# Kernel tuning notes

Hardware: AMD Instinct MI355X
Metric: run time of the kernel (lower is better)

The kernel has to match this reference:

```python
import jax, jax.numpy as jnp
import numpy as np

B, S, D = 512, 500, 128
NQ, NC, NQD, NCD = 10000, 500, 100, 100

def _glorot(key, shape):
    fan_in, fan_out = shape[0], shape[1]
    lim = np.sqrt(6.0 / (fan_in + fan_out))
    return jax.random.uniform(key, shape, jnp.float32, -lim, lim)

def setup_inputs() -> dict:
    key = jax.random.key(0)
    ks = jax.random.split(key, 24)
    inp = {
        'question_seq': jax.random.randint(ks[0], (B, S), 0, NQ),
        'concept_seq': jax.random.randint(ks[1], (B, S), 0, NC),
        'question_diff_seq': jax.random.randint(ks[2], (B, S), 0, NQD),
        'concept_diff_seq': jax.random.randint(ks[3], (B, S), 0, NCD),
        'correct_seq': jax.random.randint(ks[4], (B, S), 0, 2),
        # embedding tables
        'Eq': jax.random.normal(ks[5], (NQ, D), jnp.float32),
        'Ec': jax.random.normal(ks[6], (NC, D), jnp.float32),
        'Eqd': jax.random.normal(ks[7], (NQD, D), jnp.float32),
        'Ecd': jax.random.normal(ks[8], (NCD, D), jnp.float32),
        'Ecorr': jax.random.normal(ks[9], (2, D), jnp.float32),
        # linear layers (stored as [in, out], y = x @ W + b)
        'Wx': _glorot(ks[10], (4 * D, D)), 'bx': jnp.zeros((D,), jnp.float32),
        'Wsdf1': _glorot(ks[11], (D, D)), 'bsdf1': jnp.zeros((D,), jnp.float32),
        'Wsdf2': _glorot(ks[12], (D, D)), 'bsdf2': jnp.zeros((D,), jnp.float32),
        'Wpka1': _glorot(ks[13], (2 * D, D)), 'bpka1': jnp.zeros((D,), jnp.float32),
        'Wpka2': _glorot(ks[14], (2 * D, D)), 'bpka2': jnp.zeros((D,), jnp.float32),
        'Wki': _glorot(ks[15], (4 * D, D)), 'bki': jnp.zeros((D,), jnp.float32),
        # xavier_uniform init of h_pre (torch nn.init.xavier_uniform_ on zeros(B, D))
        'h0': _glorot(ks[16], (B, D)),
    }
    return inp

def reference(question_seq, concept_seq, question_diff_seq, concept_diff_seq,
              correct_seq, Eq, Ec, Eqd, Ecd, Ecorr, Wx, bx,
              Wsdf1, bsdf1, Wsdf2, bsdf2, Wpka1, bpka1, Wpka2, bpka2,
              Wki, bki, h0):
    # embed all sequences: [B, S, D]
    qe = Eq[question_seq]
    ce = Ec[concept_seq]
    qde = Eqd[question_diff_seq]
    cde = Ecd[concept_diff_seq]
    co = Ecorr[correct_seq]
    # x_t = generate_x_MLP(concat(...)) precomputed for all timesteps
    x_all = jnp.concatenate([qe, ce, qde, cde], axis=-1) @ Wx + bx  # [B, S, D]

    # time-major slices for scan over t = 0 .. S-2
    tm = lambda a: jnp.swapaxes(a, 0, 1)  # [S, B, D]
    xs = (tm(x_all)[:-1], tm(x_all)[1:], tm(co)[:-1], tm(qde)[:-1], tm(cde)[:-1])

    def step(h_pre, inputs):
        x_t, x_next, co_t, qd_t, cd_t = inputs
        input_sdf = x_t - h_pre
        sdf = jax.nn.sigmoid(input_sdf @ Wsdf1 + bsdf1) * jnp.tanh(input_sdf @ Wsdf2 + bsdf2)
        input_pka = jnp.concatenate([sdf, co_t], axis=-1)
        pka = jax.nn.sigmoid(input_pka @ Wpka1 + bpka1) * jnp.tanh(input_pka @ Wpka2 + bpka2)
        input_ki = jnp.concatenate([h_pre, co_t, qd_t, cd_t], axis=-1)
        gamma = jax.nn.sigmoid(input_ki @ Wki + bki)
        h = gamma * h_pre + (1.0 - gamma) * pka
        y_t = jax.nn.sigmoid(jnp.sum(x_next * h, axis=-1))  # [B]
        return h, y_t

    _, ys = jax.lax.scan(step, h0, xs)  # ys: [S-1, B]
    # y[:, S-1] is never written in the original (stays 0)
    y = jnp.concatenate([ys.T, jnp.zeros((question_seq.shape[0], 1), jnp.float32)], axis=1)
    return y
```

## Files before the change

### kernel.cpp

```cpp
#include <hip/hip_runtime.h>
#include <hip/hip_bf16.h>
#include <cstdint>
#include <cstddef>

#define BB 512
#define SS 500
#define TT 499
#define NRB 256
#define L2E 1.4426950408889634f

typedef float  f32x4  __attribute__((ext_vector_type(4)));
typedef short  bf16x8 __attribute__((ext_vector_type(8)));

static constexpr size_t OFF_TXQ   = 0;
static constexpr size_t OFF_TXC   = 5120000;
static constexpr size_t OFF_TXQD  = 5376000;
static constexpr size_t OFF_TXCD  = 5427200;
static constexpr size_t OFF_TKIQD = 5478400;
static constexpr size_t OFF_TKICD = 5529600;
static constexpr size_t OFF_TKICO = 5580800;
static constexpr size_t OFF_TP1   = 5581824;
static constexpr size_t OFF_TP2   = 5582848;
static constexpr size_t OFF_TXQ2  = 5583872;
static constexpr size_t OFF_TXC2  = 10703872;
static constexpr size_t OFF_WFRAG = 10959872;
static constexpr size_t OFF_CPK   = 11123712;
static constexpr size_t OFF_XCD   = 11254784;
static constexpr size_t OFF_KIPRE = 143375360;
static constexpr size_t OFF_YPART = 275495936;
static constexpr size_t TOTAL_WS  = 283671552;

__device__ unsigned char g_fb[TOTAL_WS];

__device__ __forceinline__ unsigned short f2bf(float f) {
    union { float f; uint32_t u; } v; v.f = f;
    uint32_t u = v.u;
    uint32_t r = u + 0x7FFFu + ((u >> 16) & 1u);
    return (unsigned short)(r >> 16);
}
__device__ __forceinline__ float fsig(float z) {
    return __builtin_amdgcn_rcpf(1.0f + __expf(-z));
}
__device__ __forceinline__ uint32_t cvtpk(float lo, float hi) {
    uint32_t r;
    asm("v_cvt_pk_bf16_f32 %0, %1, %2" : "=v"(r) : "v"(lo), "v"(hi));
    return r;
}
__device__ __forceinline__ void bar_lgkm() {
    asm volatile("s_waitcnt lgkmcnt(0)" ::: "memory");
    __builtin_amdgcn_s_barrier();
}
__device__ __forceinline__ float sum16(float x) {
    int a = __float_as_int(x);
    int b = __builtin_amdgcn_update_dpp(a, a, 0xB1, 0xF, 0xF, false);
    float s = x + __int_as_float(b);
    int c = __float_as_int(s);
    int d = __builtin_amdgcn_update_dpp(c, c, 0x4E, 0xF, 0xF, false);
    s += __int_as_float(d);
    int e = __float_as_int(s);
    int f = __builtin_amdgcn_update_dpp(e, e, 0x141, 0xF, 0xF, false);
    s += __int_as_float(f);
    int gg = __float_as_int(s);
    int hh = __builtin_amdgcn_update_dpp(gg, gg, 0x140, 0xF, 0xF, false);
    return s + __int_as_float(hh);
}

__global__ __launch_bounds__(128) void k_tables(
    const float* __restrict__ Eq, const float* __restrict__ Ec,
    const float* __restrict__ Eqd, const float* __restrict__ Ecd,
    const float* __restrict__ Ecorr,
    const float* __restrict__ Wx,  const float* __restrict__ bx,
    const float* __restrict__ Wpka1, const float* __restrict__ bpka1,
    const float* __restrict__ Wpka2, const float* __restrict__ bpka2,
    const float* __restrict__ Wki, const float* __restrict__ bki,
    float* __restrict__ Txq, float* __restrict__ Txc,
    float* __restrict__ Txqd, float* __restrict__ Txcd,
    float* __restrict__ TkiQd, float* __restrict__ TkiCd, float* __restrict__ TkiCo,
    float* __restrict__ Tp1, float* __restrict__ Tp2)
{
    int blk = blockIdx.x;
    const float* A; const float* W; const float* bias = nullptr; float* out; int row;
    float oscale = 1.0f;
    if      (blk < 10000) { A = Eq;    row = blk;          W = Wx;              bias = bx;    out = Txq;  }
    else if (blk < 10500) { A = Ec;    row = blk - 10000;  W = Wx  + 128*128;                 out = Txc;  }
    else if (blk < 10600) { A = Eqd;   row = blk - 10500;  W = Wx  + 256*128;                 out = Txqd; }
    else if (blk < 10700) { A = Ecd;   row = blk - 10600;  W = Wx  + 384*128;                 out = Txcd; }
    else if (blk < 10800) { A = Eqd;   row = blk - 10700;  W = Wki + 256*128;                 out = TkiQd;}
    else if (blk < 10900) { A = Ecd;   row = blk - 10800;  W = Wki + 384*128;                 out = TkiCd;}
    else if (blk < 10902) { A = Ecorr; row = blk - 10900;  W = Wki + 128*128;   bias = bki;   out = TkiCo;}
    else if (blk < 10904) { A = Ecorr; row = blk - 10902;  W = Wpka1 + 128*128; bias = bpka1; out = Tp1;  oscale = -L2E; }
    else                  { A = Ecorr; row = blk - 10904;  W = Wpka2 + 128*128; bias = bpka2; out = Tp2;  oscale = -2.0f*L2E; }

    __shared__ float a[128];
    int c = threadIdx.x;
    a[c] = A[row * 128 + c];
    __syncthreads();
    float acc = bias ? bias[c] : 0.0f;
    #pragma unroll 8
    for (int k = 0; k < 128; ++k) acc += a[k] * W[k * 128 + c];
    out[row * 128 + c] = acc * oscale;
}

__global__ __launch_bounds__(128) void k_tables2(
    const float* __restrict__ Wki,
    const float* __restrict__ Txq, const float* __restrict__ Txc,
    const float* __restrict__ Txqd, const float* __restrict__ Txcd,
    float* __restrict__ Txq2, float* __restrict__ Txc2,
    float* __restrict__ TkiQd, float* __restrict__ TkiCd)
{
    int blk = blockIdx.x;
    const float* A; float* out; int row; bool accum;
    if      (blk < 10000) { A = Txq;  row = blk;          out = Txq2;  accum = false; }
    else if (blk < 10500) { A = Txc;  row = blk - 10000;  out = Txc2;  accum = false; }
    else if (blk < 10600) { A = Txqd; row = blk - 10500;  out = TkiQd; accum = true;  }
    else                  { A = Txcd; row = blk - 10600;  out = TkiCd; accum = true;  }
    __shared__ float a[128];
    int c = threadIdx.x;
    a[c] = A[row * 128 + c];
    __syncthreads();
    float acc = accum ? out[row * 128 + c] : 0.0f;
    #pragma unroll 8
    for (int k = 0; k < 128; ++k) acc += a[k] * Wki[k * 128 + c];
    out[row * 128 + c] = acc;
}

__global__ __launch_bounds__(64) void k_wfrag(
    const float* __restrict__ Wsdf1, const float* __restrict__ Wsdf2,
    const float* __restrict__ Wpka1, const float* __restrict__ Wpka2,
    const float* __restrict__ Wki, unsigned short* __restrict__ wfrag)
{
    int bid = blockIdx.x;
    int m = bid >> 5, w = (bid >> 2) & 7, kt = bid & 3;
    const float* W = (m == 0) ? Wsdf1 : (m == 1) ? Wsdf2 : (m == 2) ? Wpka1 : (m == 3) ? Wpka2 : Wki;
    float sgn = (m == 0) ? -L2E : (m == 1) ? -2.0f*L2E : (m == 2) ? -L2E : (m == 3) ? -2.0f*L2E : L2E;
    int l = threadIdx.x;
    int cc = w * 16 + (l & 15);
    int k0 = kt * 32 + ((l >> 4) << 3);
    unsigned short v[8];
    #pragma unroll
    for (int j = 0; j < 8; ++j) v[j] = f2bf(sgn * W[(size_t)(k0 + j) * 128 + cc]);
    unsigned short* dst = wfrag + ((( (size_t)m * 8 + w) * 4 + kt) * 64 + l) * 8;
    #pragma unroll
    for (int j = 0; j < 8; ++j) dst[j] = v[j];
}

__global__ __launch_bounds__(256) void k_gather(
    const int* __restrict__ qs, const int* __restrict__ cs,
    const int* __restrict__ qds, const int* __restrict__ cds, const int* __restrict__ corr,
    const float* __restrict__ Txq, const float* __restrict__ Txc,
    const float* __restrict__ Txqd, const float* __restrict__ Txcd,
    const float* __restrict__ Txq2, const float* __restrict__ Txc2,
    const float* __restrict__ TkiQd, const float* __restrict__ TkiCd, const float* __restrict__ TkiCo,
    float* __restrict__ xcd, float* __restrict__ kipre, unsigned char* __restrict__ cpk)
{
    int bid = blockIdx.x;
    int t = bid >> 8, rb = bid & 255;
    int tid = threadIdx.x;
    int row = tid >> 7;
    int col = tid & 127;
    int b = rb * 2 + row;

    int iq  = qs  [(size_t)b * SS + t];
    int ic  = cs  [(size_t)b * SS + t];
    int iqd = qds [(size_t)b * SS + t];
    int icd = cds [(size_t)b * SS + t];
    int ico = corr[(size_t)b * SS + t];

    float x = Txq [(size_t)iq  * 128 + col] + Txc [(size_t)ic  * 128 + col]
            + Txqd[(size_t)iqd * 128 + col] + Txcd[(size_t)icd * 128 + col];
    float k = (Txq2 [(size_t)iq  * 128 + col] + Txc2 [(size_t)ic  * 128 + col]
             + TkiQd[(size_t)iqd * 128 + col] + TkiCd[(size_t)icd * 128 + col]
             + TkiCo[(size_t)ico * 128 + col]) * (-L2E);

    xcd  [(size_t)bid * 256 + tid] = x;
    kipre[(size_t)bid * 256 + tid] = k;

    if (tid == 0) {
        unsigned char bpk = 0;
        #pragma unroll
        for (int r = 0; r < 2; ++r)
            bpk |= (unsigned char)((corr[(size_t)(rb * 2 + r) * SS + t] & 1) << r);
        cpk[(size_t)rb * 512 + t] = bpk;
    }
}

__global__ __launch_bounds__(512, 2) void k_rec(
    const float* __restrict__ xcd, const float* __restrict__ kipre,
    const unsigned char* __restrict__ cpkg,
    const unsigned short* __restrict__ wfrag,
    const float* __restrict__ Tp1, const float* __restrict__ Tp2,
    const float* __restrict__ bsdf1, const float* __restrict__ bsdf2,
    const float* __restrict__ h0, float* __restrict__ ypart)
{
    int rb = blockIdx.x;
    int tid = threadIdx.x;
    int w = tid >> 6, l = tid & 63;
    int g = l >> 4, cl = l & 15;
    int col = w * 16 + cl;
    int row = g & 1;
    bool owner = (g < 2);

    __shared__ __align__(16) unsigned short dbuf[256];
    __shared__ __align__(16) unsigned short sbuf[256];

    bf16x8 wf[5][4];
    #pragma unroll
    for (int m = 0; m < 5; ++m)
        #pragma unroll
        for (int kt = 0; kt < 4; ++kt)
            wf[m][kt] = *(const bf16x8*)(wfrag + ((((size_t)m * 8 + w) * 4 + kt) * 64 + l) * 8);

    float bs1 = bsdf1[col] * (-L2E);
    float bs2 = bsdf2[col] * (-2.0f * L2E);
    float tp1a = Tp1[col], tp1b = Tp1[128 + col];
    float tp2a = Tp2[col], tp2b = Tp2[128 + col];

    float h = h0[(size_t)(rb * 2 + row) * 128 + col];

    char* pdw = (char*)dbuf + row * 256 + ((col * 2) ^ (row << 6));
    char* psw = (char*)sbuf + row * 256 + ((col * 2) ^ (row << 6));
    const bf16x8* prd[4]; const bf16x8* prs[4];
    int rrow = cl & 1;
    #pragma unroll
    for (int kt = 0; kt < 4; ++kt) {
        int off = rrow * 256 + ((kt * 64 + g * 16) ^ (rrow << 6));
        prd[kt] = (const bf16x8*)((char*)dbuf + off);
        prs[kt] = (const bf16x8*)((char*)sbuf + off);
    }

    const size_t TSTR = (size_t)NRB * 256;
    int eidx = row * 128 + col;
    const float* xp = xcd + (size_t)rb * 256 + eidx;
    const float* kp = kipre + (size_t)rb * 256 + eidx;
    const unsigned char* cp = cpkg + (size_t)rb * 512;

    float xn   = xp[TSTR];
    float xn2  = xp[2 * TSTR];
    float kip  = kp[0];
    float kip1 = kp[TSTR];
    unsigned char c0 = cp[0], c1v = cp[1];

    float* ypt = ypart + (size_t)rb * 16 + w * 2 + row;
    const size_t YSTR = (size_t)NRB * 16;
    bool ystore = (owner && cl == 0);

    {
        float x0 = xp[0];
        uint32_t pk = cvtpk(x0 - h, x0 - h);
        if (owner) *(unsigned short*)pdw = (unsigned short)pk;
    }
    bar_lgkm();

    #pragma unroll 2
    for (int t = 0; t < TT; ++t) {
        float xn3  = xp[(size_t)(t + 3) * TSTR];
        float kip2 = kp[(size_t)(t + 2) * TSTR];
        unsigned char c2v = cp[t + 2];

        f32x4 s1a = {bs1, bs1, bs1, bs1}, s1b = {0.f, 0.f, 0.f, 0.f};
        f32x4 s2a = {bs2, bs2, bs2, bs2}, s2b = {0.f, 0.f, 0.f, 0.f};
        f32x4 gda = {0.f, 0.f, 0.f, 0.f}, gdb = {0.f, 0.f, 0.f, 0.f};
        {
            bf16x8 d0 = *prd[0], d1 = *prd[1], d2 = *prd[2], d3 = *prd[3];
            s1a = __builtin_amdgcn_mfma_f32_16x16x32_bf16(d0, wf[0][0], s1a, 0, 0, 0);
            s2a = __builtin_amdgcn_mfma_f32_16x16x32_bf16(d0, wf[1][0], s2a, 0, 0, 0);
            gda = __builtin_amdgcn_mfma_f32_16x16x32_bf16(d0, wf[4][0], gda, 0, 0, 0);
            s1b = __builtin_amdgcn_mfma_f32_16x16x32_bf16(d2, wf[0][2], s1b, 0, 0, 0);
            s2b = __builtin_amdgcn_mfma_f32_16x16x32_bf16(d2, wf[1][2], s2b, 0, 0, 0);
            gdb = __builtin_amdgcn_mfma_f32_16x16x32_bf16(d2, wf[4][2], gdb, 0, 0, 0);
            s1a = __builtin_amdgcn_mfma_f32_16x16x32_bf16(d1, wf[0][1], s1a, 0, 0, 0);
            s2a = __builtin_amdgcn_mfma_f32_16x16x32_bf16(d1, wf[1][1], s2a, 0, 0, 0);
            gda = __builtin_amdgcn_mfma_f32_16x16x32_bf16(d1, wf[4][1], gda, 0, 0, 0);
            s1b = __builtin_amdgcn_mfma_f32_16x16x32_bf16(d3, wf[0][3], s1b, 0, 0, 0);
            s2b = __builtin_amdgcn_mfma_f32_16x16x32_bf16(d3, wf[1][3], s2b, 0, 0, 0);
            gdb = __builtin_amdgcn_mfma_f32_16x16x32_bf16(d3, wf[4][3], gdb, 0, 0, 0);
        }
        float s1v = (row ? s1a[1] : s1a[0]) + (row ? s1b[1] : s1b[0]);
        float s2v = (row ? s2a[1] : s2a[0]) + (row ? s2b[1] : s2b[0]);
        float gdv = (row ? gda[1] : gda[0]) + (row ? gdb[1] : gdb[0]);
        float gv = __builtin_amdgcn_rcpf(1.0f + __builtin_amdgcn_exp2f(gdv + kip));
        float e1 = __builtin_amdgcn_exp2f(s1v), e2 = __builtin_amdgcn_exp2f(s2v);
        float sdf = (1.0f - e2) * __builtin_amdgcn_rcpf((1.0f + e1) * (1.0f + e2));
        {
            uint32_t pk = cvtpk(sdf, sdf);
            if (owner) *(unsigned short*)psw = (unsigned short)pk;
        }
        bar_lgkm();

        f32x4 p1a = {0.f, 0.f, 0.f, 0.f}, p1b = {0.f, 0.f, 0.f, 0.f};
        f32x4 p2a = {0.f, 0.f, 0.f, 0.f}, p2b = {0.f, 0.f, 0.f, 0.f};
        {
            bf16x8 f0 = *prs[0], f1 = *prs[1], f2 = *prs[2], f3 = *prs[3];
            p1a = __builtin_amdgcn_mfma_f32_16x16x32_bf16(f0, wf[2][0], p1a, 0, 0, 0);
            p2a = __builtin_amdgcn_mfma_f32_16x16x32_bf16(f0, wf[3][0], p2a, 0, 0, 0);
            p1b = __builtin_amdgcn_mfma_f32_16x16x32_bf16(f2, wf[2][2], p1b, 0, 0, 0);
            p2b = __builtin_amdgcn_mfma_f32_16x16x32_bf16(f2, wf[3][2], p2b, 0, 0, 0);
            p1a = __builtin_amdgcn_mfma_f32_16x16x32_bf16(f1, wf[2][1], p1a, 0, 0, 0);
            p2a = __builtin_amdgcn_mfma_f32_16x16x32_bf16(f1, wf[3][1], p2a, 0, 0, 0);
            p1b = __builtin_amdgcn_mfma_f32_16x16x32_bf16(f3, wf[2][3], p1b, 0, 0, 0);
            p2b = __builtin_amdgcn_mfma_f32_16x16x32_bf16(f3, wf[3][3], p2b, 0, 0, 0);
        }
        float p1v = (row ? p1a[1] : p1a[0]) + (row ? p1b[1] : p1b[0]);
        float p2v = (row ? p2a[1] : p2a[0]) + (row ? p2b[1] : p2b[0]);
        unsigned int myb = (((unsigned int)c0) >> row) & 1u;
        float t1 = myb ? tp1b : tp1a;
        float t2 = myb ? tp2b : tp2a;
        float e1p = __builtin_amdgcn_exp2f(p1v + t1), e2p = __builtin_amdgcn_exp2f(p2v + t2);
        float pka = (1.0f - e2p) * __builtin_amdgcn_rcpf((1.0f + e1p) * (1.0f + e2p));
        h = gv * (h - pka) + pka;

        {
            uint32_t pk = cvtpk(xn - h, xn - h);
            if (owner) *(unsigned short*)pdw = (unsigned short)pk;
        }
        float yv = sum16(xn * h);
        if (ystore) ypt[0] = yv;
        ypt += YSTR;
        bar_lgkm();

        xn = xn2; xn2 = xn3; kip = kip1; kip1 = kip2; c0 = c1v; c1v = c2v;
    }
}

__global__ __launch_bounds__(256) void k_yfinal(const float* __restrict__ ypart, float* __restrict__ y)
{
    int id = blockIdx.x * 256 + threadIdx.x;
    if (id >= BB * SS) return;
    int b = id / SS, t = id - b * SS;
    if (t == TT) { y[id] = 0.0f; return; }
    int rb = b >> 1, r = b & 1;
    const float* base = ypart + (size_t)t * NRB * 16 + (size_t)rb * 16 + r;
    float s = 0.0f;
    #pragma unroll
    for (int w = 0; w < 8; ++w) s += base[w * 2];
    y[id] = fsig(s);
}

extern "C" void kernel_launch(void* const* d_in, const int* in_sizes, int n_in,
                              void* d_out, int out_size, void* d_ws, size_t ws_size,
                              hipStream_t stream) {
    const int* qs    = (const int*)d_in[0];
    const int* cs    = (const int*)d_in[1];
    const int* qds   = (const int*)d_in[2];
    const int* cds   = (const int*)d_in[3];
    const int* corr  = (const int*)d_in[4];
    const float* Eq    = (const float*)d_in[5];
    const float* Ec    = (const float*)d_in[6];
    const float* Eqd   = (const float*)d_in[7];
    const float* Ecd   = (const float*)d_in[8];
    const float* Ecorr = (const float*)d_in[9];
    const float* Wx    = (const float*)d_in[10];
    const float* bx    = (const float*)d_in[11];
    const float* Wsdf1 = (const float*)d_in[12];
    const float* bsdf1 = (const float*)d_in[13];
    const float* Wsdf2 = (const float*)d_in[14];
    const float* bsdf2 = (const float*)d_in[15];
    const float* Wpka1 = (const float*)d_in[16];
    const float* bpka1 = (const float*)d_in[17];
    const float* Wpka2 = (const float*)d_in[18];
    const float* bpka2 = (const float*)d_in[19];
    const float* Wki   = (const float*)d_in[20];
    const float* bki   = (const float*)d_in[21];
    const float* h0    = (const float*)d_in[22];

    char* base;
    if (ws_size >= TOTAL_WS) {
        base = (char*)d_ws;
    } else {
        void* p = nullptr;
        hipGetSymbolAddress(&p, HIP_SYMBOL(g_fb));
        base = (char*)p;
    }

    float* Txq   = (float*)(base + OFF_TXQ);
    float* Txc   = (float*)(base + OFF_TXC);
    float* Txqd  = (float*)(base + OFF_TXQD);
    float* Txcd  = (float*)(base + OFF_TXCD);
    float* TkiQd = (float*)(base + OFF_TKIQD);
    float* TkiCd = (float*)(base + OFF_TKICD);
    float* TkiCo = (float*)(base + OFF_TKICO);
    float* Tp1   = (float*)(base + OFF_TP1);
    float* Tp2   = (float*)(base + OFF_TP2);
    float* Txq2  = (float*)(base + OFF_TXQ2);
    float* Txc2  = (float*)(base + OFF_TXC2);
    unsigned short* wfrag = (unsigned short*)(base + OFF_WFRAG);
    unsigned char*  cpk   = (unsigned char*)(base + OFF_CPK);
    float* xcd   = (float*)(base + OFF_XCD);
    float* kipre = (float*)(base + OFF_KIPRE);
    float* ypart = (float*)(base + OFF_YPART);

    k_tables<<<10906, 128, 0, stream>>>(Eq, Ec, Eqd, Ecd, Ecorr, Wx, bx,
                                        Wpka1, bpka1, Wpka2, bpka2, Wki, bki,
                                        Txq, Txc, Txqd, Txcd, TkiQd, TkiCd, TkiCo, Tp1, Tp2);
    k_tables2<<<10700, 128, 0, stream>>>(Wki, Txq, Txc, Txqd, Txcd, Txq2, Txc2, TkiQd, TkiCd);
    k_wfrag<<<160, 64, 0, stream>>>(Wsdf1, Wsdf2, Wpka1, Wpka2, Wki, wfrag);
    k_gather<<<SS * NRB, 256, 0, stream>>>(qs, cs, qds, cds, corr,
                                           Txq, Txc, Txqd, Txcd, Txq2, Txc2,
                                           TkiQd, TkiCd, TkiCo, xcd, kipre, cpk);
    k_rec<<<NRB, 512, 0, stream>>>(xcd, kipre, cpk, wfrag, Tp1, Tp2,
                                   bsdf1, bsdf2, h0, ypart);
    k_yfinal<<<(BB * SS + 255) / 256, 256, 0, stream>>>(ypart, (float*)d_out);
}
```

Baseline: 550.0 us.

## Skew the two batch rows by half a step so their phases overlap

The recurrence kernel now handles its two batch rows as separate streams, A and B, offset by half a timestep. In each barrier-delimited phase, one row's sdf/gate matmuls run next to the other row's pka matmuls, and each row has its own LDS buffers. The aim is to give each phase independent MFMA and transcendental chains to interleave, hiding latency in the serial per-step dependency. The cost is that each MFMA now carries only one meaningful row instead of packing both, so MFMA count per step roughly doubles, and the loop unroll drops to 1.

```diff
diff --git a/kernel.cpp b/kernel.cpp
--- a/kernel.cpp
+++ b/kernel.cpp
@@ -11,6 +11,8 @@
 
 typedef float  f32x4  __attribute__((ext_vector_type(4)));
 typedef short  bf16x8 __attribute__((ext_vector_type(8)));
+
+#define MFMA16(A, B, C) __builtin_amdgcn_mfma_f32_16x16x32_bf16((A), (B), (C), 0, 0, 0)
 
 static constexpr size_t OFF_TXQ   = 0;
 static constexpr size_t OFF_TXC   = 5120000;
@@ -197,11 +199,13 @@
     int w = tid >> 6, l = tid & 63;
     int g = l >> 4, cl = l & 15;
     int col = w * 16 + cl;
-    int row = g & 1;
-    bool owner = (g < 2);
-
-    __shared__ __align__(16) unsigned short dbuf[256];
-    __shared__ __align__(16) unsigned short sbuf[256];
+    bool owner = (g == 0);
+    bool ystore = (l == 0);
+
+    __shared__ __align__(16) unsigned short dbufA[128];
+    __shared__ __align__(16) unsigned short sbufA[128];
+    __shared__ __align__(16) unsigned short dbufB[128];
+    __shared__ __align__(16) unsigned short sbufB[128];
 
     bf16x8 wf[5][4];
     #pragma unroll
@@ -215,110 +219,160 @@
     float tp1a = Tp1[col], tp1b = Tp1[128 + col];
     float tp2a = Tp2[col], tp2b = Tp2[128 + col];
 
-    float h = h0[(size_t)(rb * 2 + row) * 128 + col];
-
-    char* pdw = (char*)dbuf + row * 256 + ((col * 2) ^ (row << 6));
-    char* psw = (char*)sbuf + row * 256 + ((col * 2) ^ (row << 6));
-    const bf16x8* prd[4]; const bf16x8* prs[4];
-    int rrow = cl & 1;
-    #pragma unroll
-    for (int kt = 0; kt < 4; ++kt) {
-        int off = rrow * 256 + ((kt * 64 + g * 16) ^ (rrow << 6));
-        prd[kt] = (const bf16x8*)((char*)dbuf + off);
-        prs[kt] = (const bf16x8*)((char*)sbuf + off);
-    }
+    float hA = h0[(size_t)(rb * 2 + 0) * 128 + col];
+    float hB = h0[(size_t)(rb * 2 + 1) * 128 + col];
+
+    char* pdwA = (char*)dbufA + col * 2;
+    char* pswA = (char*)sbufA + col * 2;
+    char* pdwB = (char*)dbufB + col * 2;
+    char* pswB = (char*)sbufB + col * 2;
+    const char* rdA = (const char*)dbufA + g * 16;
+    const char* rsA = (const char*)sbufA + g * 16;
+    const char* rdB = (const char*)dbufB + g * 16;
+    const char* rsB = (const char*)sbufB + g * 16;
 
     const size_t TSTR = (size_t)NRB * 256;
-    int eidx = row * 128 + col;
-    const float* xp = xcd + (size_t)rb * 256 + eidx;
-    const float* kp = kipre + (size_t)rb * 256 + eidx;
+    const float* xpA = xcd + (size_t)rb * 256 + col;
+    const float* xpB = xpA + 128;
+    const float* kpA = kipre + (size_t)rb * 256 + col;
+    const float* kpB = kpA + 128;
     const unsigned char* cp = cpkg + (size_t)rb * 512;
 
-    float xn   = xp[TSTR];
-    float xn2  = xp[2 * TSTR];
-    float kip  = kp[0];
-    float kip1 = kp[TSTR];
-    unsigned char c0 = cp[0], c1v = cp[1];
-
-    float* ypt = ypart + (size_t)rb * 16 + w * 2 + row;
+    float xA0 = xpA[0], xB0 = xpB[0];
+    float kipA0 = kpA[0];
+    float kipB0 = kpB[0];
+    float xA1 = xpA[TSTR], xB1 = xpB[TSTR];
+    float kipB1 = kpB[TSTR];
+    unsigned char cpk0 = cp[0];
+    unsigned int cA0 = cpk0 & 1u, cB0 = (cpk0 >> 1) & 1u;
+
+    float* yptA = ypart + ((size_t)rb * 8 + w) * 2;
+    float* yptB = yptA + 1;
     const size_t YSTR = (size_t)NRB * 16;
-    bool ystore = (owner && cl == 0);
-
-    {
-        float x0 = xp[0];
-        uint32_t pk = cvtpk(x0 - h, x0 - h);
-        if (owner) *(unsigned short*)pdw = (unsigned short)pk;
+
+    if (owner) {
+        *(unsigned short*)pdwA = (unsigned short)cvtpk(xA0 - hA, xA0 - hA);
+        *(unsigned short*)pdwB = (unsigned short)cvtpk(xB0 - hB, xB0 - hB);
     }
     bar_lgkm();
-
-    #pragma unroll 2
-    for (int t = 0; t < TT; ++t) {
-        float xn3  = xp[(size_t)(t + 3) * TSTR];
-        float kip2 = kp[(size_t)(t + 2) * TSTR];
-        unsigned char c2v = cp[t + 2];
-
-        f32x4 s1a = {bs1, bs1, bs1, bs1}, s1b = {0.f, 0.f, 0.f, 0.f};
-        f32x4 s2a = {bs2, bs2, bs2, bs2}, s2b = {0.f, 0.f, 0.f, 0.f};
-        f32x4 gda = {0.f, 0.f, 0.f, 0.f}, gdb = {0.f, 0.f, 0.f, 0.f};
-        {
-            bf16x8 d0 = *prd[0], d1 = *prd[1], d2 = *prd[2], d3 = *prd[3];
-            s1a = __builtin_amdgcn_mfma_f32_16x16x32_bf16(d0, wf[0][0], s1a, 0, 0, 0);
-            s2a = __builtin_amdgcn_mfma_f32_16x16x32_bf16(d0, wf[1][0], s2a, 0, 0, 0);
-            gda = __builtin_amdgcn_mfma_f32_16x16x32_bf16(d0, wf[4][0], gda, 0, 0, 0);
-            s1b = __builtin_amdgcn_mfma_f32_16x16x32_bf16(d2, wf[0][2], s1b, 0, 0, 0);
-            s2b = __builtin_amdgcn_mfma_f32_16x16x32_bf16(d2, wf[1][2], s2b, 0, 0, 0);
-            gdb = __builtin_amdgcn_mfma_f32_16x16x32_bf16(d2, wf[4][2], gdb, 0, 0, 0);
-            s1a = __builtin_amdgcn_mfma_f32_16x16x32_bf16(d1, wf[0][1], s1a, 0, 0, 0);
-            s2a = __builtin_amdgcn_mfma_f32_16x16x32_bf16(d1, wf[1][1], s2a, 0, 0, 0);
-            gda = __builtin_amdgcn_mfma_f32_16x16x32_bf16(d1, wf[4][1], gda, 0, 0, 0);
-            s1b = __builtin_amdgcn_mfma_f32_16x16x32_bf16(d3, wf[0][3], s1b, 0, 0, 0);
-            s2b = __builtin_amdgcn_mfma_f32_16x16x32_bf16(d3, wf[1][3], s2b, 0, 0, 0);
-            gdb = __builtin_amdgcn_mfma_f32_16x16x32_bf16(d3, wf[4][3], gdb, 0, 0, 0);
-        }
-        float s1v = (row ? s1a[1] : s1a[0]) + (row ? s1b[1] : s1b[0]);
-        float s2v = (row ? s2a[1] : s2a[0]) + (row ? s2b[1] : s2b[0]);
-        float gdv = (row ? gda[1] : gda[0]) + (row ? gdb[1] : gdb[0]);
-        float gv = __builtin_amdgcn_rcpf(1.0f + __builtin_amdgcn_exp2f(gdv + kip));
+    float gvA, gvB;
+    {
+        bf16x8 b0 = *(const bf16x8*)(rdB +   0);
+        bf16x8 b1 = *(const bf16x8*)(rdB +  64);
+        bf16x8 b2 = *(const bf16x8*)(rdB + 128);
+        bf16x8 b3 = *(const bf16x8*)(rdB + 192);
+        f32x4 s1a = {bs1,bs1,bs1,bs1}, s1b = {0.f,0.f,0.f,0.f};
+        f32x4 s2a = {bs2,bs2,bs2,bs2}, s2b = {0.f,0.f,0.f,0.f};
+        f32x4 gda = {0.f,0.f,0.f,0.f}, gdb = {0.f,0.f,0.f,0.f};
+        s1a = MFMA16(b0, wf[0][0], s1a); s2a = MFMA16(b0, wf[1][0], s2a); gda = MFMA16(b0, wf[4][0], gda);
+        s1b = MFMA16(b2, wf[0][2], s1b); s2b = MFMA16(b2, wf[1][2], s2b); gdb = MFMA16(b2, wf[4][2], gdb);
+        s1a = MFMA16(b1, wf[0][1], s1a); s2a = MFMA16(b1, wf[1][1], s2a); gda = MFMA16(b1, wf[4][1], gda);
+        s1b = MFMA16(b3, wf[0][3], s1b); s2b = MFMA16(b3, wf[1][3], s2b); gdb = MFMA16(b3, wf[4][3], gdb);
+        float s1v = s1a[0] + s1b[0], s2v = s2a[0] + s2b[0], gdv = gda[0] + gdb[0];
+        gvB = __builtin_amdgcn_rcpf(1.0f + __builtin_amdgcn_exp2f(gdv + kipB0));
         float e1 = __builtin_amdgcn_exp2f(s1v), e2 = __builtin_amdgcn_exp2f(s2v);
         float sdf = (1.0f - e2) * __builtin_amdgcn_rcpf((1.0f + e1) * (1.0f + e2));
+        if (owner) *(unsigned short*)pswB = (unsigned short)cvtpk(sdf, sdf);
+    }
+    bar_lgkm();
+
+    #pragma unroll 1
+    for (int t = 0; t < TT; ++t) {
+        float xA1n   = xpA[(size_t)(t + 2) * TSTR];
+        float xB1n   = xpB[(size_t)(t + 2) * TSTR];
+        float kipA0n = kpA[(size_t)(t + 1) * TSTR];
+        float kipB1n = kpB[(size_t)(t + 2) * TSTR];
+        unsigned char cpkN = cp[t + 1];
+
         {
-            uint32_t pk = cvtpk(sdf, sdf);
-            if (owner) *(unsigned short*)psw = (unsigned short)pk;
+            bf16x8 a0 = *(const bf16x8*)(rdA +   0);
+            bf16x8 a1 = *(const bf16x8*)(rdA +  64);
+            bf16x8 a2 = *(const bf16x8*)(rdA + 128);
+            bf16x8 a3 = *(const bf16x8*)(rdA + 192);
+            bf16x8 f0 = *(const bf16x8*)(rsB +   0);
+            bf16x8 f1 = *(const bf16x8*)(rsB +  64);
+            bf16x8 f2 = *(const bf16x8*)(rsB + 128);
+            bf16x8 f3 = *(const bf16x8*)(rsB + 192);
+            f32x4 s1a = {bs1,bs1,bs1,bs1}, s1b = {0.f,0.f,0.f,0.f};
+            f32x4 s2a = {bs2,bs2,bs2,bs2}, s2b = {0.f,0.f,0.f,0.f};
+            f32x4 gda = {0.f,0.f,0.f,0.f}, gdb = {0.f,0.f,0.f,0.f};
+            f32x4 p1a = {0.f,0.f,0.f,0.f}, p1b = {0.f,0.f,0.f,0.f};
+            f32x4 p2a = {0.f,0.f,0.f,0.f}, p2b = {0.f,0.f,0.f,0.f};
+            s1a = MFMA16(a0, wf[0][0], s1a); p1a = MFMA16(f0, wf[2][0], p1a);
+            s2a = MFMA16(a0, wf[1][0], s2a); p2a = MFMA16(f0, wf[3][0], p2a);
+            gda = MFMA16(a0, wf[4][0], gda);
+            s1b = MFMA16(a2, wf[0][2], s1b); p1b = MFMA16(f2, wf[2][2], p1b);
+            s2b = MFMA16(a2, wf[1][2], s2b); p2b = MFMA16(f2, wf[3][2], p2b);
+            gdb = MFMA16(a2, wf[4][2], gdb);
+            s1a = MFMA16(a1, wf[0][1], s1a); p1a = MFMA16(f1, wf[2][1], p1a);
+            s2a = MFMA16(a1, wf[1][1], s2a); p2a = MFMA16(f1, wf[3][1], p2a);
+            gda = MFMA16(a1, wf[4][1], gda);
+            s1b = MFMA16(a3, wf[0][3], s1b); p1b = MFMA16(f3, wf[2][3], p1b);
+            s2b = MFMA16(a3, wf[1][3], s2b); p2b = MFMA16(f3, wf[3][3], p2b);
+            gdb = MFMA16(a3, wf[4][3], gdb);
+            float s1v = s1a[0] + s1b[0], s2v = s2a[0] + s2b[0], gdv = gda[0] + gdb[0];
+            gvA = __builtin_amdgcn_rcpf(1.0f + __builtin_amdgcn_exp2f(gdv + kipA0));
+            float e1 = __builtin_amdgcn_exp2f(s1v), e2 = __builtin_amdgcn_exp2f(s2v);
+            float sdf = (1.0f - e2) * __builtin_amdgcn_rcpf((1.0f + e1) * (1.0f + e2));
+            if (owner) *(unsigned short*)pswA = (unsigned short)cvtpk(sdf, sdf);
+            float p1v = p1a[0] + p1b[0], p2v = p2a[0] + p2b[0];
+            float t1 = cB0 ? tp1b : tp1a;
+            float t2 = cB0 ? tp2b : tp2a;
+            float e1p = __builtin_amdgcn_exp2f(p1v + t1), e2p = __builtin_amdgcn_exp2f(p2v + t2);
+            float pka = (1.0f - e2p) * __builtin_amdgcn_rcpf((1.0f + e1p) * (1.0f + e2p));
+            hB = gvB * (hB - pka) + pka;
+            if (owner) *(unsigned short*)pdwB = (unsigned short)cvtpk(xB1 - hB, xB1 - hB);
+            float yB = sum16(xB1 * hB);
+            if (ystore) yptB[0] = yB;
         }
         bar_lgkm();
 
-        f32x4 p1a = {0.f, 0.f, 0.f, 0.f}, p1b = {0.f, 0.f, 0.f, 0.f};
-        f32x4 p2a = {0.f, 0.f, 0.f, 0.f}, p2b = {0.f, 0.f, 0.f, 0.f};
         {
-            bf16x8 f0 = *prs[0], f1 = *prs[1], f2 = *prs[2], f3 = *prs[3];
-            p1a = __builtin_amdgcn_mfma_f32_16x16x32_bf16(f0, wf[2][0], p1a, 0, 0, 0);
-            p2a = __builtin_amdgcn_mfma_f32_16x16x32_bf16(f0, wf[3][0], p2a, 0, 0, 0);
-            p1b = __builtin_amdgcn_mfma_f32_16x16x32_bf16(f2, wf[2][2], p1b, 0, 0, 0);
-            p2b = __builtin_amdgcn_mfma_f32_16x16x32_bf16(f2, wf[3][2], p2b, 0, 0, 0);
-            p1a = __builtin_amdgcn_mfma_f32_16x16x32_bf16(f1, wf[2][1], p1a, 0, 0, 0);
-            p2a = __builtin_amdgcn_mfma_f32_16x16x32_bf16(f1, wf[3][1], p2a, 0, 0, 0);
-            p1b = __builtin_amdgcn_mfma_f32_16x16x32_bf16(f3, wf[2][3], p1b, 0, 0, 0);
-            p2b = __builtin_amdgcn_mfma_f32_16x16x32_bf16(f3, wf[3][3], p2b, 0, 0, 0);
+            bf16x8 a0 = *(const bf16x8*)(rsA +   0);
+            bf16x8 a1 = *(const bf16x8*)(rsA +  64);
+            bf16x8 a2 = *(const bf16x8*)(rsA + 128);
+            bf16x8 a3 = *(const bf16x8*)(rsA + 192);
+            bf16x8 f0 = *(const bf16x8*)(rdB +   0);
+            bf16x8 f1 = *(const bf16x8*)(rdB +  64);
+            bf16x8 f2 = *(const bf16x8*)(rdB + 128);
+            bf16x8 f3 = *(const bf16x8*)(rdB + 192);
+            f32x4 p1a = {0.f,0.f,0.f,0.f}, p1b = {0.f,0.f,0.f,0.f};
+            f32x4 p2a = {0.f,0.f,0.f,0.f}, p2b = {0.f,0.f,0.f,0.f};
+            f32x4 s1a = {bs1,bs1,bs1,bs1}, s1b = {0.f,0.f,0.f,0.f};
+            f32x4 s2a = {bs2,bs2,bs2,bs2}, s2b = {0.f,0.f,0.f,0.f};
+            f32x4 gda = {0.f,0.f,0.f,0.f}, gdb = {0.f,0.f,0.f,0.f};
+            p1a = MFMA16(a0, wf[2][0], p1a); s1a = MFMA16(f0, wf[0][0], s1a);
+            p2a = MFMA16(a0, wf[3][0], p2a); s2a = MFMA16(f0, wf[1][0], s2a);
+            gda = MFMA16(f0, wf[4][0], gda);
+            p1b = MFMA16(a2, wf[2][2], p1b); s1b = MFMA16(f2, wf[0][2], s1b);
+            p2b = MFMA16(a2, wf[3][2], p2b); s2b = MFMA16(f2, wf[1][2], s2b);
+            gdb = MFMA16(f2, wf[4][2], gdb);
+            p1a = MFMA16(a1, wf[2][1], p1a); s1a = MFMA16(f1, wf[0][1], s1a);
+            p2a = MFMA16(a1, wf[3][1], p2a); s2a = MFMA16(f1, wf[1][1], s2a);
+            gda = MFMA16(f1, wf[4][1], gda);
+            p1b = MFMA16(a3, wf[2][3], p1b); s1b = MFMA16(f3, wf[0][3], s1b);
+            p2b = MFMA16(a3, wf[3][3], p2b); s2b = MFMA16(f3, wf[1][3], s2b);
+            gdb = MFMA16(f3, wf[4][3], gdb);
+            float p1v = p1a[0] + p1b[0], p2v = p2a[0] + p2b[0];
+            float t1 = cA0 ? tp1b : tp1a;
+            float t2 = cA0 ? tp2b : tp2a;
+            float e1p = __builtin_amdgcn_exp2f(p1v + t1), e2p = __builtin_amdgcn_exp2f(p2v + t2);
+            float pka = (1.0f - e2p) * __builtin_amdgcn_rcpf((1.0f + e1p) * (1.0f + e2p));
+            hA = gvA * (hA - pka) + pka;
+            if (owner) *(unsigned short*)pdwA = (unsigned short)cvtpk(xA1 - hA, xA1 - hA);
+            float yA = sum16(xA1 * hA);
+            if (ystore) yptA[0] = yA;
+            float s1v = s1a[0] + s1b[0], s2v = s2a[0] + s2b[0], gdv = gda[0] + gdb[0];
+            gvB = __builtin_amdgcn_rcpf(1.0f + __builtin_amdgcn_exp2f(gdv + kipB1));
+            float e1 = __builtin_amdgcn_exp2f(s1v), e2 = __builtin_amdgcn_exp2f(s2v);
+            float sdf = (1.0f - e2) * __builtin_amdgcn_rcpf((1.0f + e1) * (1.0f + e2));
+            if (owner) *(unsigned short*)pswB = (unsigned short)cvtpk(sdf, sdf);
         }
-        float p1v = (row ? p1a[1] : p1a[0]) + (row ? p1b[1] : p1b[0]);
-        float p2v = (row ? p2a[1] : p2a[0]) + (row ? p2b[1] : p2b[0]);
-        unsigned int myb = (((unsigned int)c0) >> row) & 1u;
-        float t1 = myb ? tp1b : tp1a;
-        float t2 = myb ? tp2b : tp2a;
-        float e1p = __builtin_amdgcn_exp2f(p1v + t1), e2p = __builtin_amdgcn_exp2f(p2v + t2);
-        float pka = (1.0f - e2p) * __builtin_amdgcn_rcpf((1.0f + e1p) * (1.0f + e2p));
-        h = gv * (h - pka) + pka;
-
-        {
-            uint32_t pk = cvtpk(xn - h, xn - h);
-            if (owner) *(unsigned short*)pdw = (unsigned short)pk;
-        }
-        float yv = sum16(xn * h);
-        if (ystore) ypt[0] = yv;
-        ypt += YSTR;
         bar_lgkm();
 
-        xn = xn2; xn2 = xn3; kip = kip1; kip1 = kip2; c0 = c1v; c1v = c2v;
+        yptA += YSTR; yptB += YSTR;
+        xA1 = xA1n; xB1 = xB1n; kipA0 = kipA0n; kipB1 = kipB1n;
+        cA0 = cpkN & 1u; cB0 = (cpkN >> 1) & 1u;
     }
 }
 
@@ -328,8 +382,8 @@
     if (id >= BB * SS) return;
     int b = id / SS, t = id - b * SS;
     if (t == TT) { y[id] = 0.0f; return; }
-    int rb = b >> 1, r = b & 1;
-    const float* base = ypart + (size_t)t * NRB * 16 + (size_t)rb * 16 + r;
+    int rb = b >> 1, pair = b & 1;
+    const float* base = ypart + (size_t)t * NRB * 16 + (size_t)rb * 16 + pair;
     float s = 0.0f;
     #pragma unroll
     for (int w = 0; w < 8; ++w) s += base[w * 2];
```

Measured after the change: 899.4 us. +63.5%, slower.

## Fuse embedding gather into recurrent kernel with interleaved x/ki tables

Applied to the files above, without the earlier changes.

Removes the separate gather kernel that materialised per-timestep x and ki-preactivation arrays (about 260MB of writes and reads). Tables now store x and ki contributions interleaved as float2 so the recurrent kernel gathers both with one load per table and prefetches indices two steps ahead. The scaling by -log2(e) is folded into the table build. The cost is dependent index-then-table loads inside the serial timestep loop, which must be hidden by the prefetch distance.

```diff
diff --git a/kernel.cpp b/kernel.cpp
--- a/kernel.cpp
+++ b/kernel.cpp
@@ -12,23 +12,20 @@
 typedef float  f32x4  __attribute__((ext_vector_type(4)));
 typedef short  bf16x8 __attribute__((ext_vector_type(8)));
 
-static constexpr size_t OFF_TXQ   = 0;
-static constexpr size_t OFF_TXC   = 5120000;
-static constexpr size_t OFF_TXQD  = 5376000;
-static constexpr size_t OFF_TXCD  = 5427200;
-static constexpr size_t OFF_TKIQD = 5478400;
-static constexpr size_t OFF_TKICD = 5529600;
-static constexpr size_t OFF_TKICO = 5580800;
-static constexpr size_t OFF_TP1   = 5581824;
-static constexpr size_t OFF_TP2   = 5582848;
-static constexpr size_t OFF_TXQ2  = 5583872;
-static constexpr size_t OFF_TXC2  = 10703872;
-static constexpr size_t OFF_WFRAG = 10959872;
-static constexpr size_t OFF_CPK   = 11123712;
-static constexpr size_t OFF_XCD   = 11254784;
-static constexpr size_t OFF_KIPRE = 143375360;
-static constexpr size_t OFF_YPART = 275495936;
-static constexpr size_t TOTAL_WS  = 283671552;
+#define MFMA16(A, B, C) __builtin_amdgcn_mfma_f32_16x16x32_bf16((A), (B), (C), 0, 0, 0)
+
+static constexpr size_t OFF_TQ    = 0;
+static constexpr size_t OFF_TC    = 10240000;
+static constexpr size_t OFF_TQD   = 10752000;
+static constexpr size_t OFF_TCD   = 10854400;
+static constexpr size_t OFF_TCOK  = 10956800;
+static constexpr size_t OFF_TP1   = 10957824;
+static constexpr size_t OFF_TP2   = 10958848;
+static constexpr size_t OFF_TMPA  = 10959872;
+static constexpr size_t OFF_TMPB  = 11011072;
+static constexpr size_t OFF_WFRAG = 11062272;
+static constexpr size_t OFF_YPART = 11226112;
+static constexpr size_t TOTAL_WS  = 19401728;
 
 __device__ unsigned char g_fb[TOTAL_WS];
 
@@ -73,21 +70,22 @@
     const float* __restrict__ Wpka1, const float* __restrict__ bpka1,
     const float* __restrict__ Wpka2, const float* __restrict__ bpka2,
     const float* __restrict__ Wki, const float* __restrict__ bki,
-    float* __restrict__ Txq, float* __restrict__ Txc,
-    float* __restrict__ Txqd, float* __restrict__ Txcd,
-    float* __restrict__ TkiQd, float* __restrict__ TkiCd, float* __restrict__ TkiCo,
-    float* __restrict__ Tp1, float* __restrict__ Tp2)
+    float* __restrict__ TQ, float* __restrict__ TC,
+    float* __restrict__ TQD, float* __restrict__ TCD,
+    float* __restrict__ TCOk, float* __restrict__ Tp1, float* __restrict__ Tp2,
+    float* __restrict__ tmpA, float* __restrict__ tmpB)
 {
     int blk = blockIdx.x;
     const float* A; const float* W; const float* bias = nullptr; float* out; int row;
+    int ostride = 1;
     float oscale = 1.0f;
-    if      (blk < 10000) { A = Eq;    row = blk;          W = Wx;              bias = bx;    out = Txq;  }
-    else if (blk < 10500) { A = Ec;    row = blk - 10000;  W = Wx  + 128*128;                 out = Txc;  }
-    else if (blk < 10600) { A = Eqd;   row = blk - 10500;  W = Wx  + 256*128;                 out = Txqd; }
-    else if (blk < 10700) { A = Ecd;   row = blk - 10600;  W = Wx  + 384*128;                 out = Txcd; }
-    else if (blk < 10800) { A = Eqd;   row = blk - 10700;  W = Wki + 256*128;                 out = TkiQd;}
-    else if (blk < 10900) { A = Ecd;   row = blk - 10800;  W = Wki + 384*128;                 out = TkiCd;}
-    else if (blk < 10902) { A = Ecorr; row = blk - 10900;  W = Wki + 128*128;   bias = bki;   out = TkiCo;}
+    if      (blk < 10000) { A = Eq;    row = blk;          W = Wx;              bias = bx;    out = TQ;   ostride = 2; }
+    else if (blk < 10500) { A = Ec;    row = blk - 10000;  W = Wx  + 128*128;                 out = TC;   ostride = 2; }
+    else if (blk < 10600) { A = Eqd;   row = blk - 10500;  W = Wx  + 256*128;                 out = TQD;  ostride = 2; }
+    else if (blk < 10700) { A = Ecd;   row = blk - 10600;  W = Wx  + 384*128;                 out = TCD;  ostride = 2; }
+    else if (blk < 10800) { A = Eqd;   row = blk - 10700;  W = Wki + 256*128;                 out = tmpA; }
+    else if (blk < 10900) { A = Ecd;   row = blk - 10800;  W = Wki + 384*128;                 out = tmpB; }
+    else if (blk < 10902) { A = Ecorr; row = blk - 10900;  W = Wki + 128*128;   bias = bki;   out = TCOk; oscale = -L2E; }
     else if (blk < 10904) { A = Ecorr; row = blk - 10902;  W = Wpka1 + 128*128; bias = bpka1; out = Tp1;  oscale = -L2E; }
     else                  { A = Ecorr; row = blk - 10904;  W = Wpka2 + 128*128; bias = bpka2; out = Tp2;  oscale = -2.0f*L2E; }
 
@@ -98,30 +96,29 @@
     float acc = bias ? bias[c] : 0.0f;
     #pragma unroll 8
     for (int k = 0; k < 128; ++k) acc += a[k] * W[k * 128 + c];
-    out[row * 128 + c] = acc * oscale;
+    out[(size_t)(row * 128 + c) * ostride] = acc * oscale;
 }
 
 __global__ __launch_bounds__(128) void k_tables2(
     const float* __restrict__ Wki,
-    const float* __restrict__ Txq, const float* __restrict__ Txc,
-    const float* __restrict__ Txqd, const float* __restrict__ Txcd,
-    float* __restrict__ Txq2, float* __restrict__ Txc2,
-    float* __restrict__ TkiQd, float* __restrict__ TkiCd)
+    float* __restrict__ TQ, float* __restrict__ TC,
+    float* __restrict__ TQD, float* __restrict__ TCD,
+    const float* __restrict__ tmpA, const float* __restrict__ tmpB)
 {
     int blk = blockIdx.x;
-    const float* A; float* out; int row; bool accum;
-    if      (blk < 10000) { A = Txq;  row = blk;          out = Txq2;  accum = false; }
-    else if (blk < 10500) { A = Txc;  row = blk - 10000;  out = Txc2;  accum = false; }
-    else if (blk < 10600) { A = Txqd; row = blk - 10500;  out = TkiQd; accum = true;  }
-    else                  { A = Txcd; row = blk - 10600;  out = TkiCd; accum = true;  }
+    float* base2; const float* tmp = nullptr; int row;
+    if      (blk < 10000) { row = blk;          base2 = TQ  + (size_t)row * 256; }
+    else if (blk < 10500) { row = blk - 10000;  base2 = TC  + (size_t)row * 256; }
+    else if (blk < 10600) { row = blk - 10500;  base2 = TQD + (size_t)row * 256; tmp = tmpA + (size_t)row * 128; }
+    else                  { row = blk - 10600;  base2 = TCD + (size_t)row * 256; tmp = tmpB + (size_t)row * 128; }
     __shared__ float a[128];
     int c = threadIdx.x;
-    a[c] = A[row * 128 + c];
+    a[c] = base2[c * 2];
     __syncthreads();
-    float acc = accum ? out[row * 128 + c] : 0.0f;
+    float acc = tmp ? tmp[c] : 0.0f;
     #pragma unroll 8
     for (int k = 0; k < 128; ++k) acc += a[k] * Wki[k * 128 + c];
-    out[row * 128 + c] = acc;
+    base2[c * 2 + 1] = acc * (-L2E);
 }
 
 __global__ __launch_bounds__(64) void k_wfrag(
@@ -144,49 +141,12 @@
     for (int j = 0; j < 8; ++j) dst[j] = v[j];
 }
 
-__global__ __launch_bounds__(256) void k_gather(
+__global__ __launch_bounds__(512, 2) void k_rec(
     const int* __restrict__ qs, const int* __restrict__ cs,
     const int* __restrict__ qds, const int* __restrict__ cds, const int* __restrict__ corr,
-    const float* __restrict__ Txq, const float* __restrict__ Txc,
-    const float* __restrict__ Txqd, const float* __restrict__ Txcd,
-    const float* __restrict__ Txq2, const float* __restrict__ Txc2,
-    const float* __restrict__ TkiQd, const float* __restrict__ TkiCd, const float* __restrict__ TkiCo,
-    float* __restrict__ xcd, float* __restrict__ kipre, unsigned char* __restrict__ cpk)
-{
-    int bid = blockIdx.x;
-    int t = bid >> 8, rb = bid & 255;
-    int tid = threadIdx.x;
-    int row = tid >> 7;
-    int col = tid & 127;
-    int b = rb * 2 + row;
-
-    int iq  = qs  [(size_t)b * SS + t];
-    int ic  = cs  [(size_t)b * SS + t];
-    int iqd = qds [(size_t)b * SS + t];
-    int icd = cds [(size_t)b * SS + t];
-    int ico = corr[(size_t)b * SS + t];
-
-    float x = Txq [(size_t)iq  * 128 + col] + Txc [(size_t)ic  * 128 + col]
-            + Txqd[(size_t)iqd * 128 + col] + Txcd[(size_t)icd * 128 + col];
-    float k = (Txq2 [(size_t)iq  * 128 + col] + Txc2 [(size_t)ic  * 128 + col]
-             + TkiQd[(size_t)iqd * 128 + col] + TkiCd[(size_t)icd * 128 + col]
-             + TkiCo[(size_t)ico * 128 + col]) * (-L2E);
-
-    xcd  [(size_t)bid * 256 + tid] = x;
-    kipre[(size_t)bid * 256 + tid] = k;
-
-    if (tid == 0) {
-        unsigned char bpk = 0;
-        #pragma unroll
-        for (int r = 0; r < 2; ++r)
-            bpk |= (unsigned char)((corr[(size_t)(rb * 2 + r) * SS + t] & 1) << r);
-        cpk[(size_t)rb * 512 + t] = bpk;
-    }
-}
-
-__global__ __launch_bounds__(512, 2) void k_rec(
-    const float* __restrict__ xcd, const float* __restrict__ kipre,
-    const unsigned char* __restrict__ cpkg,
+    const float2* __restrict__ TQ, const float2* __restrict__ TC,
+    const float2* __restrict__ TQD, const float2* __restrict__ TCD,
+    const float* __restrict__ TCOk,
     const unsigned short* __restrict__ wfrag,
     const float* __restrict__ Tp1, const float* __restrict__ Tp2,
     const float* __restrict__ bsdf1, const float* __restrict__ bsdf2,
@@ -228,57 +188,60 @@
         prs[kt] = (const bf16x8*)((char*)sbuf + off);
     }
 
-    const size_t TSTR = (size_t)NRB * 256;
-    int eidx = row * 128 + col;
-    const float* xp = xcd + (size_t)rb * 256 + eidx;
-    const float* kp = kipre + (size_t)rb * 256 + eidx;
-    const unsigned char* cp = cpkg + (size_t)rb * 512;
-
-    float xn   = xp[TSTR];
-    float xn2  = xp[2 * TSTR];
-    float kip  = kp[0];
-    float kip1 = kp[TSTR];
-    unsigned char c0 = cp[0], c1v = cp[1];
+    int boff = (rb * 2 + row) * SS;
 
     float* ypt = ypart + (size_t)rb * 16 + w * 2 + row;
     const size_t YSTR = (size_t)NRB * 16;
     bool ystore = (owner && cl == 0);
 
+    float x1, kip0, kip1; unsigned int c0, c1;
     {
-        float x0 = xp[0];
+        int o0 = boff;
+        int iq = qs[o0], ic = cs[o0], iqd = qds[o0], icd = cds[o0], ico = corr[o0];
+        float2 q = TQ[(size_t)iq * 128 + col], c_ = TC[(size_t)ic * 128 + col];
+        float2 qd = TQD[(size_t)iqd * 128 + col], cd = TCD[(size_t)icd * 128 + col];
+        float co = TCOk[(size_t)ico * 128 + col];
+        float x0 = q.x + c_.x + qd.x + cd.x;
+        kip0 = q.y + c_.y + qd.y + cd.y + co;
+        c0 = (unsigned int)ico & 1u;
         uint32_t pk = cvtpk(x0 - h, x0 - h);
         if (owner) *(unsigned short*)pdw = (unsigned short)pk;
     }
+    {
+        int o1 = boff + 1;
+        int iq = qs[o1], ic = cs[o1], iqd = qds[o1], icd = cds[o1], ico = corr[o1];
+        float2 q = TQ[(size_t)iq * 128 + col], c_ = TC[(size_t)ic * 128 + col];
+        float2 qd = TQD[(size_t)iqd * 128 + col], cd = TCD[(size_t)icd * 128 + col];
+        float co = TCOk[(size_t)ico * 128 + col];
+        x1 = q.x + c_.x + qd.x + cd.x;
+        kip1 = q.y + c_.y + qd.y + cd.y + co;
+        c1 = (unsigned int)ico & 1u;
+    }
     bar_lgkm();
 
     #pragma unroll 2
     for (int t = 0; t < TT; ++t) {
-        float xn3  = xp[(size_t)(t + 3) * TSTR];
-        float kip2 = kp[(size_t)(t + 2) * TSTR];
-        unsigned char c2v = cp[t + 2];
+        int tp = t + 2; tp = (tp > 499) ? 499 : tp;
+        int op = boff + tp;
+        int iq = qs[op], ic = cs[op], iqd = qds[op], icd = cds[op], ico = corr[op];
+        float2 gq = TQ[(size_t)iq * 128 + col], gc = TC[(size_t)ic * 128 + col];
+        float2 gqd = TQD[(size_t)iqd * 128 + col], gcd = TCD[(size_t)icd * 128 + col];
+        float gco = TCOk[(size_t)ico * 128 + col];
 
         f32x4 s1a = {bs1, bs1, bs1, bs1}, s1b = {0.f, 0.f, 0.f, 0.f};
         f32x4 s2a = {bs2, bs2, bs2, bs2}, s2b = {0.f, 0.f, 0.f, 0.f};
         f32x4 gda = {0.f, 0.f, 0.f, 0.f}, gdb = {0.f, 0.f, 0.f, 0.f};
         {
             bf16x8 d0 = *prd[0], d1 = *prd[1], d2 = *prd[2], d3 = *prd[3];
-            s1a = __builtin_amdgcn_mfma_f32_16x16x32_bf16(d0, wf[0][0], s1a, 0, 0, 0);
-            s2a = __builtin_amdgcn_mfma_f32_16x16x32_bf16(d0, wf[1][0], s2a, 0, 0, 0);
-            gda = __builtin_amdgcn_mfma_f32_16x16x32_bf16(d0, wf[4][0], gda, 0, 0, 0);
-            s1b = __builtin_amdgcn_mfma_f32_16x16x32_bf16(d2, wf[0][2], s1b, 0, 0, 0);
-            s2b = __builtin_amdgcn_mfma_f32_16x16x32_bf16(d2, wf[1][2], s2b, 0, 0, 0);
-            gdb = __builtin_amdgcn_mfma_f32_16x16x32_bf16(d2, wf[4][2], gdb, 0, 0, 0);
-            s1a = __builtin_amdgcn_mfma_f32_16x16x32_bf16(d1, wf[0][1], s1a, 0, 0, 0);
-            s2a = __builtin_amdgcn_mfma_f32_16x16x32_bf16(d1, wf[1][1], s2a, 0, 0, 0);
-            gda = __builtin_amdgcn_mfma_f32_16x16x32_bf16(d1, wf[4][1], gda, 0, 0, 0);
-            s1b = __builtin_amdgcn_mfma_f32_16x16x32_bf16(d3, wf[0][3], s1b, 0, 0, 0);
-            s2b = __builtin_amdgcn_mfma_f32_16x16x32_bf16(d3, wf[1][3], s2b, 0, 0, 0);
-            gdb = __builtin_amdgcn_mfma_f32_16x16x32_bf16(d3, wf[4][3], gdb, 0, 0, 0);
+            s1a = MFMA16(d0, wf[0][0], s1a); s2a = MFMA16(d0, wf[1][0], s2a); gda = MFMA16(d0, wf[4][0], gda);
+            s1b = MFMA16(d2, wf[0][2], s1b); s2b = MFMA16(d2, wf[1][2], s2b); gdb = MFMA16(d2, wf[4][2], gdb);
+            s1a = MFMA16(d1, wf[0][1], s1a); s2a = MFMA16(d1, wf[1][1], s2a); gda = MFMA16(d1, wf[4][1], gda);
+            s1b = MFMA16(d3, wf[0][3], s1b); s2b = MFMA16(d3, wf[1][3], s2b); gdb = MFMA16(d3, wf[4][3], gdb);
         }
         float s1v = (row ? s1a[1] : s1a[0]) + (row ? s1b[1] : s1b[0]);
         float s2v = (row ? s2a[1] : s2a[0]) + (row ? s2b[1] : s2b[0]);
         float gdv = (row ? gda[1] : gda[0]) + (row ? gdb[1] : gdb[0]);
-        float gv = __builtin_amdgcn_rcpf(1.0f + __builtin_amdgcn_exp2f(gdv + kip));
+        float gv = __builtin_amdgcn_rcpf(1.0f + __builtin_amdgcn_exp2f(gdv + kip0));
         float e1 = __builtin_amdgcn_exp2f(s1v), e2 = __builtin_amdgcn_exp2f(s2v);
         float sdf = (1.0f - e2) * __builtin_amdgcn_rcpf((1.0f + e1) * (1.0f + e2));
         {
@@ -291,34 +254,33 @@
         f32x4 p2a = {0.f, 0.f, 0.f, 0.f}, p2b = {0.f, 0.f, 0.f, 0.f};
         {
             bf16x8 f0 = *prs[0], f1 = *prs[1], f2 = *prs[2], f3 = *prs[3];
-            p1a = __builtin_amdgcn_mfma_f32_16x16x32_bf16(f0, wf[2][0], p1a, 0, 0, 0);
-            p2a = __builtin_amdgcn_mfma_f32_16x16x32_bf16(f0, wf[3][0], p2a, 0, 0, 0);
-            p1b = __builtin_amdgcn_mfma_f32_16x16x32_bf16(f2, wf[2][2], p1b, 0, 0, 0);
-            p2b = __builtin_amdgcn_mfma_f32_16x16x32_bf16(f2, wf[3][2], p2b, 0, 0, 0);
-            p1a = __builtin_amdgcn_mfma_f32_16x16x32_bf16(f1, wf[2][1], p1a, 0, 0, 0);
-            p2a = __builtin_amdgcn_mfma_f32_16x16x32_bf16(f1, wf[3][1], p2a, 0, 0, 0);
-            p1b = __builtin_amdgcn_mfma_f32_16x16x32_bf16(f3, wf[2][3], p1b, 0, 0, 0);
-            p2b = __builtin_amdgcn_mfma_f32_16x16x32_bf16(f3, wf[3][3], p2b, 0, 0, 0);
+            p1a = MFMA16(f0, wf[2][0], p1a); p2a = MFMA16(f0, wf[3][0], p2a);
+            p1b = MFMA16(f2, wf[2][2], p1b); p2b = MFMA16(f2, wf[3][2], p2b);
+            p1a = MFMA16(f1, wf[2][1], p1a); p2a = MFMA16(f1, wf[3][1], p2a);
+            p1b = MFMA16(f3, wf[2][3], p1b); p2b = MFMA16(f3, wf[3][3], p2b);
         }
         float p1v = (row ? p1a[1] : p1a[0]) + (row ? p1b[1] : p1b[0]);
         float p2v = (row ? p2a[1] : p2a[0]) + (row ? p2b[1] : p2b[0]);
-        unsigned int myb = (((unsigned int)c0) >> row) & 1u;
-        float t1 = myb ? tp1b : tp1a;
-        float t2 = myb ? tp2b : tp2a;
+        float t1 = c0 ? tp1b : tp1a;
+        float t2 = c0 ? tp2b : tp2a;
         float e1p = __builtin_amdgcn_exp2f(p1v + t1), e2p = __builtin_amdgcn_exp2f(p2v + t2);
         float pka = (1.0f - e2p) * __builtin_amdgcn_rcpf((1.0f + e1p) * (1.0f + e2p));
         h = gv * (h - pka) + pka;
 
         {
-            uint32_t pk = cvtpk(xn - h, xn - h);
+            uint32_t pk = cvtpk(x1 - h, x1 - h);
             if (owner) *(unsigned short*)pdw = (unsigned short)pk;
         }
-        float yv = sum16(xn * h);
+        float yv = sum16(x1 * h);
         if (ystore) ypt[0] = yv;
         ypt += YSTR;
         bar_lgkm();
 
-        xn = xn2; xn2 = xn3; kip = kip1; kip1 = kip2; c0 = c1v; c1v = c2v;
+        x1 = gq.x + gc.x + gqd.x + gcd.x;
+        kip0 = kip1;
+        kip1 = gq.y + gc.y + gqd.y + gcd.y + gco;
+        c0 = c1;
+        c1 = (unsigned int)ico & 1u;
     }
 }
 
@@ -328,8 +290,8 @@
     if (id >= BB * SS) return;
     int b = id / SS, t = id - b * SS;
     if (t == TT) { y[id] = 0.0f; return; }
-    int rb = b >> 1, r = b & 1;
-    const float* base = ypart + (size_t)t * NRB * 16 + (size_t)rb * 16 + r;
+    int rb = b >> 1, pair = b & 1;
+    const float* base = ypart + (size_t)t * NRB * 16 + (size_t)rb * 16 + pair;
     float s = 0.0f;
     #pragma unroll
     for (int w = 0; w < 8; ++w) s += base[w * 2];
@@ -372,32 +334,26 @@
         base = (char*)p;
     }
 
-    float* Txq   = (float*)(base + OFF_TXQ);
-    float* Txc   = (float*)(base + OFF_TXC);
-    float* Txqd  = (float*)(base + OFF_TXQD);
-    float* Txcd  = (float*)(base + OFF_TXCD);
-    float* TkiQd = (float*)(base + OFF_TKIQD);
-    float* TkiCd = (float*)(base + OFF_TKICD);
-    float* TkiCo = (float*)(base + OFF_TKICO);
+    float* TQ    = (float*)(base + OFF_TQ);
+    float* TC    = (float*)(base + OFF_TC);
+    float* TQD   = (float*)(base + OFF_TQD);
+    float* TCD   = (float*)(base + OFF_TCD);
+    float* TCOk  = (float*)(base + OFF_TCOK);
     float* Tp1   = (float*)(base + OFF_TP1);
     float* Tp2   = (float*)(base + OFF_TP2);
-    float* Txq2  = (float*)(base + OFF_TXQ2);
-    float* Txc2  = (float*)(base + OFF_TXC2);
+    float* tmpA  = (float*)(base + OFF_TMPA);
+    float* tmpB  = (float*)(base + OFF_TMPB);
     unsigned short* wfrag = (unsigned short*)(base + OFF_WFRAG);
-    unsigned char*  cpk   = (unsigned char*)(base + OFF_CPK);
-    float* xcd   = (float*)(base + OFF_XCD);
-    float* kipre = (float*)(base + OFF_KIPRE);
     float* ypart = (float*)(base + OFF_YPART);
 
     k_tables<<<10906, 128, 0, stream>>>(Eq, Ec, Eqd, Ecd, Ecorr, Wx, bx,
                                         Wpka1, bpka1, Wpka2, bpka2, Wki, bki,
-                                        Txq, Txc, Txqd, Txcd, TkiQd, TkiCd, TkiCo, Tp1, Tp2);
-    k_tables2<<<10700, 128, 0, stream>>>(Wki, Txq, Txc, Txqd, Txcd, Txq2, Txc2, TkiQd, TkiCd);
+                                        TQ, TC, TQD, TCD, TCOk, Tp1, Tp2, tmpA, tmpB);
+    k_tables2<<<10700, 128, 0, stream>>>(Wki, TQ, TC, TQD, TCD, tmpA, tmpB);
     k_wfrag<<<160, 64, 0, stream>>>(Wsdf1, Wsdf2, Wpka1, Wpka2, Wki, wfrag);
-    k_gather<<<SS * NRB, 256, 0, stream>>>(qs, cs, qds, cds, corr,
-                                           Txq, Txc, Txqd, Txcd, Txq2, Txc2,
-                                           TkiQd, TkiCd, TkiCo, xcd, kipre, cpk);
-    k_rec<<<NRB, 512, 0, stream>>>(xcd, kipre, cpk, wfrag, Tp1, Tp2,
-                                   bsdf1, bsdf2, h0, ypart);
+    k_rec<<<NRB, 512, 0, stream>>>(qs, cs, qds, cds, corr,
+                                   (const float2*)TQ, (const float2*)TC,
+                                   (const float2*)TQD, (const float2*)TCD, TCOk,
+                                   wfrag, Tp1, Tp2, bsdf1, bsdf2, h0, ypart);
     k_yfinal<<<(BB * SS + 255) / 256, 256, 0, stream>>>(ypart, (float*)d_out);
 }
```

After: 530.9 us. -3.5%, faster.
